# Optimization experiments

Hardware: AMD Instinct MI355X
Metric: run time of the kernel (lower is better)

Reference implementation:

```python
import jax, jax.numpy as jnp
import numpy as np

B, C, H, W = 32, 256, 32, 32
C8 = C // 8


def setup_inputs() -> dict:
    key = jax.random.key(0)
    ks = jax.random.split(key, 8)
    s = 1.0 / np.sqrt(C)
    return {
        "x": jax.random.normal(ks[0], (B, C, H, W), dtype=jnp.float32),
        "Wq": jax.random.normal(ks[1], (C8, C), dtype=jnp.float32) * s,
        "bq": jax.random.normal(ks[2], (C8,), dtype=jnp.float32) * s,
        "Wk": jax.random.normal(ks[3], (C8, C), dtype=jnp.float32) * s,
        "bk": jax.random.normal(ks[4], (C8,), dtype=jnp.float32) * s,
        "Wv": jax.random.normal(ks[5], (C, C), dtype=jnp.float32) * s,
        "bv": jax.random.normal(ks[6], (C,), dtype=jnp.float32) * s,
        "gamma": jax.random.normal(ks[7], (1,), dtype=jnp.float32) * 0.1,
    }


def reference(x, Wq, bq, Wk, bk, Wv, bv, gamma):
    b, c, h, w = x.shape
    n = h * w
    xf = x.reshape(b, c, n)  # [B, C, N]
    # 1x1 convs == per-pixel linear projections
    q = jnp.einsum('dc,bcn->bnd', Wq, xf) + bq            # [B, N, C/8]
    k = jnp.einsum('dc,bcn->bdn', Wk, xf) + bk[:, None]    # [B, C/8, N]
    v = jnp.einsum('dc,bcn->bdn', Wv, xf) + bv[:, None]    # [B, C, N]
    energy = jnp.einsum('bnd,bdm->bnm', q, k)              # [B, N, N], no scaling (as in source)
    attn = jax.nn.softmax(energy, axis=-1)                 # softmax over keys
    # out[:, :, i] = sum_j V[:, :, j] * attn[i, j]
    out = jnp.einsum('bdn,bmn->bdm', v, attn)              # [B, C, N]
    out = out.reshape(b, c, h, w)
    return gamma * out + x
```

## Files before the change

kernel.cpp:

```cpp
#include <hip/hip_runtime.h>
#include <math.h>

#define BB 32
#define CC 256
#define CQ 32
#define NN 1024

typedef short bf16x8 __attribute__((ext_vector_type(8)));
typedef float f32x4  __attribute__((ext_vector_type(4)));
typedef unsigned short u16;

__device__ __forceinline__ u16 f2bf(float f) {
    unsigned u = __float_as_uint(f);
    u = (u + 0x7FFFu + ((u >> 16) & 1u)) >> 16;
    return (u16)u;
}

__global__ void wpack_kernel(const float* __restrict__ Wq,
                             const float* __restrict__ Wk,
                             const float* __restrict__ Wv,
                             u16* __restrict__ wfrag)
{
    const int o = blockIdx.x * 256 + threadIdx.x;
    const int j    = o & 7;
    const int lane = (o >> 3) & 63;
    const int kc   = (o >> 9) & 7;
    const int rt   = o >> 12;
    const int row  = rt * 16 + (lane & 15);
    const int col  = kc * 32 + (lane >> 4) * 8 + j;
    const float v = (row < 32) ? Wq[row * 256 + col]
                  : (row < 64) ? Wk[(row - 32) * 256 + col]
                               : Wv[(row - 64) * 256 + col];
    wfrag[o] = f2bf(v);
}

struct QSmem {
    union {
        u16 xs[64][268];
        u16 osv[CC][72];
    };
    u16 osqk[64][72];
};

__global__ __launch_bounds__(256, 2) void qkv_kernel(
    const float* __restrict__ x, const u16* __restrict__ wfrag,
    const float* __restrict__ bq, const float* __restrict__ bk,
    const float* __restrict__ bv,
    u16* __restrict__ qt, u16* __restrict__ kt, u16* __restrict__ vv)
{
    __shared__ QSmem sm;
    const int b = blockIdx.y, n0 = blockIdx.x * 64;
    const int t = threadIdx.x;
    const int lane = t & 63, w = t >> 6;
    const int quad = lane >> 4, c16 = lane & 15;

    {
        const float* xb = x + (size_t)b * CC * NN + n0;
        const int n2 = 2 * (lane & 31);
        const int cr = w * 2 + (lane >> 5);
        float2 f[32];
#pragma unroll
        for (int it = 0; it < 32; ++it)
            f[it] = *(const float2*)(xb + (size_t)(it * 8 + cr) * NN + n2);
#pragma unroll
        for (int it = 0; it < 32; ++it) {
            const int c = it * 8 + cr;
            sm.xs[n2 + 0][c] = f2bf(f[it].x);
            sm.xs[n2 + 1][c] = f2bf(f[it].y);
        }
    }
    __syncthreads();

    f32x4 acc[5][4];
#pragma unroll
    for (int i = 0; i < 5; ++i)
#pragma unroll
        for (int j = 0; j < 4; ++j) acc[i][j] = (f32x4){0.f, 0.f, 0.f, 0.f};

#pragma unroll 2
    for (int k = 0; k < 8; ++k) {
        const int c0 = k * 32;
        bf16x8 wa[5], xb[4];
#pragma unroll
        for (int rs = 0; rs < 5; ++rs)
            wa[rs] = *(const bf16x8*)&wfrag[(size_t)(((w * 5 + rs) * 8 + k) * 64 + lane) * 8];
#pragma unroll
        for (int ns = 0; ns < 4; ++ns) {
            const short4 a = *(const short4*)&sm.xs[ns * 16 + c16][c0 + quad * 8];
            const short4 b2 = *(const short4*)&sm.xs[ns * 16 + c16][c0 + quad * 8 + 4];
            bf16x8 v;
            v[0] = a.x; v[1] = a.y; v[2] = a.z; v[3] = a.w;
            v[4] = b2.x; v[5] = b2.y; v[6] = b2.z; v[7] = b2.w;
            xb[ns] = v;
        }
#pragma unroll
        for (int rs = 0; rs < 5; ++rs)
#pragma unroll
            for (int ns = 0; ns < 4; ++ns)
                acc[rs][ns] = __builtin_amdgcn_mfma_f32_16x16x32_bf16(
                    wa[rs], xb[ns], acc[rs][ns], 0, 0, 0);
    }

    __syncthreads();

#pragma unroll
    for (int rs = 0; rs < 5; ++rs) {
#pragma unroll
        for (int r = 0; r < 4; ++r) {
            const int rg = w * 80 + rs * 16 + quad * 4 + r;
            const float bias = (rg < 32) ? bq[rg] : (rg < 64) ? bk[rg - 32] : bv[rg - 64];
#pragma unroll
            for (int ns = 0; ns < 4; ++ns) {
                const int n = ns * 16 + c16;
                const u16 h = f2bf(acc[rs][ns][r] + bias);
                if (rg < 64) sm.osqk[n][rg] = h;
                else         sm.osv[rg - 64][n] = h;
            }
        }
    }
    __syncthreads();

    {
        u16* dst = (w >= 2) ? kt : qt;
        const int dof = (w >= 2) ? 32 : 0;
        const int wl = w & 1;
        const size_t base = ((size_t)b * NN + n0) * CQ;
#pragma unroll
        for (int it = 0; it < 4; ++it) {
            const int o = wl * 2048 + it * 512 + lane * 8;
            const int n = o >> 5, d = o & 31;
            const bf16x8 v = *(const bf16x8*)&sm.osqk[n][d + dof];
            *(bf16x8*)&dst[base + o] = v;
        }
    }
#pragma unroll
    for (int it = 0; it < 8; ++it) {
        const int o = it * 2048 + t * 8;
        const int c = o >> 6, n = o & 63;
        const bf16x8 v = *(const bf16x8*)&sm.osv[c][n];
        *(bf16x8*)&vv[((size_t)b * CC + c) * NN + n0 + n] = v;
    }
}

__global__ __launch_bounds__(256, 2) void attn_kernel(
    const u16* __restrict__ qt, const u16* __restrict__ kt,
    const u16* __restrict__ vv, const float* __restrict__ x,
    const float* __restrict__ gamma_p, float* __restrict__ out)
{
    __shared__ u16 ps16[2][64][72];

    const int bid  = blockIdx.x;
    const int xcd  = bid & 7;
    const int slot = bid >> 3;
    const int b    = (xcd << 2) | (slot >> 4);
    const int m0   = (slot & 15) * 64;

    const int t = threadIdx.x, lane = t & 63, w = t >> 6;
    const int quad = lane >> 4, c16 = lane & 15;
    const int ch   = c16 >> 3;
    const int c7   = c16 & 7;
    const int qkey = (c16 >> 2) & 3;

    const bf16x8 qa = *(const bf16x8*)&qt[((size_t)b * NN + m0 + w * 16 + c16) * CQ + quad * 8];

    bf16x8 ones;
#pragma unroll
    for (int j = 0; j < 8; ++j) ones[j] = (short)0x3F80;

    f32x4 accO[4][4];
    f32x4 lsum[4];
#pragma unroll
    for (int i = 0; i < 4; ++i) {
        lsum[i] = (f32x4){0.f, 0.f, 0.f, 0.f};
#pragma unroll
        for (int j = 0; j < 4; ++j) accO[i][j] = (f32x4){0.f, 0.f, 0.f, 0.f};
    }

    const u16* vbase = vv + (size_t)b * CC * NN;
    const u16* kbase = kt + (size_t)b * NN * CQ;

    bf16x8 kb[4];
#pragma unroll
    for (int s = 0; s < 4; ++s)
        kb[s] = *(const bf16x8*)&kbase[(size_t)(s * 16 + c16) * CQ + quad * 8];

    bf16x8 vaA[4][2], vaB[4][2];
#pragma unroll
    for (int cs = 0; cs < 4; ++cs)
#pragma unroll
        for (int kc = 0; kc < 2; ++kc)
            vaA[cs][kc] = *(const bf16x8*)&vbase[
                (size_t)(w * 64 + cs * 16 + c16) * NN + kc * 32 + quad * 8];

    auto STEP = [&](int step, bf16x8 (&vc)[4][2], bf16x8 (&vn)[4][2]) {
        const int nbase = step * 64;
        u16* psb = &ps16[step & 1][0][0];

        f32x4 accS[4];
#pragma unroll
        for (int s = 0; s < 4; ++s)
            accS[s] = __builtin_amdgcn_mfma_f32_16x16x32_bf16(
                qa, kb[s], (f32x4){0.f, 0.f, 0.f, 0.f}, 0, 0, 0);

        const int rowb = w * 16 + quad * 4;
#pragma unroll
        for (int r = 0; r < 4; ++r)
#pragma unroll
            for (int s = 0; s < 4; ++s) {
                const int nb = (2 * s + ch) ^ quad;
                psb[(rowb + r) * 72 + nb * 8 + c7] = f2bf(__expf(accS[s][r]));
            }

        if (step < 15) {
#pragma unroll
            for (int s = 0; s < 4; ++s)
                kb[s] = *(const bf16x8*)&kbase[(size_t)(nbase + 64 + s * 16 + c16) * CQ + quad * 8];
        }

        __syncthreads();

        if (step < 15) {
#pragma unroll
            for (int cs = 0; cs < 4; ++cs)
#pragma unroll
                for (int kc = 0; kc < 2; ++kc)
                    vn[cs][kc] = *(const bf16x8*)&vbase[
                        (size_t)(w * 64 + cs * 16 + c16) * NN + nbase + 64 + kc * 32 + quad * 8];
        }

#pragma unroll
        for (int ms = 0; ms < 4; ++ms) {
            bf16x8 pb[2];
#pragma unroll
            for (int kc = 0; kc < 2; ++kc)
                pb[kc] = *(const bf16x8*)&psb[(ms * 16 + c16) * 72
                                              + (4 * kc + (quad ^ qkey)) * 8];
            lsum[ms] = __builtin_amdgcn_mfma_f32_16x16x32_bf16(ones, pb[0], lsum[ms], 0, 0, 0);
            lsum[ms] = __builtin_amdgcn_mfma_f32_16x16x32_bf16(ones, pb[1], lsum[ms], 0, 0, 0);
#pragma unroll
            for (int cs = 0; cs < 4; ++cs) {
#pragma unroll
                for (int kc = 0; kc < 2; ++kc)
                    accO[cs][ms] = __builtin_amdgcn_mfma_f32_16x16x32_bf16(
                        vc[cs][kc], pb[kc], accO[cs][ms], 0, 0, 0);
            }
        }
    };

    for (int it = 0; it < 8; ++it) {
        STEP(2 * it,     vaA, vaB);
        STEP(2 * it + 1, vaB, vaA);
    }

    const float gamma = gamma_p[0];
#pragma unroll
    for (int ms = 0; ms < 4; ++ms) {
        const float inv = gamma / lsum[ms][0];
        const int m = m0 + ms * 16 + c16;
#pragma unroll
        for (int cs = 0; cs < 4; ++cs) {
            const int cbase = w * 64 + cs * 16 + quad * 4;
#pragma unroll
            for (int r = 0; r < 4; ++r) {
                const size_t idx = ((size_t)b * CC + cbase + r) * NN + m;
                out[idx] = accO[cs][ms][r] * inv + x[idx];
            }
        }
    }
}

extern "C" void kernel_launch(void* const* d_in, const int* in_sizes, int n_in,
                              void* d_out, int out_size, void* d_ws, size_t ws_size,
                              hipStream_t stream)
{
    const float* x  = (const float*)d_in[0];
    const float* Wq = (const float*)d_in[1];
    const float* bq = (const float*)d_in[2];
    const float* Wk = (const float*)d_in[3];
    const float* bk = (const float*)d_in[4];
    const float* Wv = (const float*)d_in[5];
    const float* bv = (const float*)d_in[6];
    const float* gm = (const float*)d_in[7];
    float* out = (float*)d_out;

    u16* qt    = (u16*)d_ws;
    u16* kt    = qt + (size_t)BB * NN * CQ;
    u16* vv    = kt + (size_t)BB * NN * CQ;
    u16* wfrag = vv + (size_t)BB * CC * NN;

    wpack_kernel<<<320, 256, 0, stream>>>(Wq, Wk, Wv, wfrag);
    dim3 grid(16, BB);
    qkv_kernel<<<grid, 256, 0, stream>>>(x, wfrag, bq, bk, bv, qt, kt, vv);
    attn_kernel<<<512, 256, 0, stream>>>(qt, kt, vv, x, gm, out);
}
```

Measured before the change: 155.9 us.

## Split attention block across 8 waves and pack bf16 conversions

Doubles the attention kernel's block to 512 threads so each wave owns 32 output channels instead of 64, and the S-tile computation is split across waves by key half. The row sum is computed by one wave per row group and shared through LDS. Exp results are now converted with the packed v_cvt_pk_bf16_f32 instruction. The V register double-buffering is dropped in favour of loading V at the start of each step. This reduces register pressure to raise occupancy, at the cost of more sync participants and less explicit prefetch.

```diff
diff --git a/kernel.cpp b/kernel.cpp
--- a/kernel.cpp
+++ b/kernel.cpp
@@ -14,6 +14,12 @@
     unsigned u = __float_as_uint(f);
     u = (u + 0x7FFFu + ((u >> 16) & 1u)) >> 16;
     return (u16)u;
+}
+
+__device__ __forceinline__ unsigned cvt_pk_bf16(float lo, float hi) {
+    unsigned r;
+    asm("v_cvt_pk_bf16_f32 %0, %1, %2" : "=v"(r) : "v"(lo), "v"(hi));
+    return r;
 }
 
 __global__ void wpack_kernel(const float* __restrict__ Wq,
@@ -142,12 +148,13 @@
     }
 }
 
-__global__ __launch_bounds__(256, 2) void attn_kernel(
+__global__ __launch_bounds__(512, 4) void attn_kernel(
     const u16* __restrict__ qt, const u16* __restrict__ kt,
     const u16* __restrict__ vv, const float* __restrict__ x,
     const float* __restrict__ gamma_p, float* __restrict__ out)
 {
     __shared__ u16 ps16[2][64][72];
+    __shared__ float lsh[64];
 
     const int bid  = blockIdx.x;
     const int xcd  = bid & 7;
@@ -160,106 +167,106 @@
     const int ch   = c16 >> 3;
     const int c7   = c16 & 7;
     const int qkey = (c16 >> 2) & 3;
-
-    const bf16x8 qa = *(const bf16x8*)&qt[((size_t)b * NN + m0 + w * 16 + c16) * CQ + quad * 8];
+    const int sm   = w & 3;
+    const int sh   = w >> 2;
+    const int ms0  = w & 3;
+
+    const bf16x8 qa = *(const bf16x8*)&qt[((size_t)b * NN + m0 + sm * 16 + c16) * CQ + quad * 8];
 
     bf16x8 ones;
 #pragma unroll
     for (int j = 0; j < 8; ++j) ones[j] = (short)0x3F80;
 
-    f32x4 accO[4][4];
-    f32x4 lsum[4];
-#pragma unroll
-    for (int i = 0; i < 4; ++i) {
-        lsum[i] = (f32x4){0.f, 0.f, 0.f, 0.f};
-#pragma unroll
-        for (int j = 0; j < 4; ++j) accO[i][j] = (f32x4){0.f, 0.f, 0.f, 0.f};
-    }
+    f32x4 accO[2][4];
+    f32x4 lsum = (f32x4){0.f, 0.f, 0.f, 0.f};
+#pragma unroll
+    for (int cs = 0; cs < 2; ++cs)
+#pragma unroll
+        for (int j = 0; j < 4; ++j) accO[cs][j] = (f32x4){0.f, 0.f, 0.f, 0.f};
 
     const u16* vbase = vv + (size_t)b * CC * NN;
     const u16* kbase = kt + (size_t)b * NN * CQ;
 
-    bf16x8 kb[4];
-#pragma unroll
-    for (int s = 0; s < 4; ++s)
-        kb[s] = *(const bf16x8*)&kbase[(size_t)(s * 16 + c16) * CQ + quad * 8];
-
-    bf16x8 vaA[4][2], vaB[4][2];
-#pragma unroll
-    for (int cs = 0; cs < 4; ++cs)
-#pragma unroll
-        for (int kc = 0; kc < 2; ++kc)
-            vaA[cs][kc] = *(const bf16x8*)&vbase[
-                (size_t)(w * 64 + cs * 16 + c16) * NN + kc * 32 + quad * 8];
-
-    auto STEP = [&](int step, bf16x8 (&vc)[4][2], bf16x8 (&vn)[4][2]) {
+    bf16x8 kb[2];
+#pragma unroll
+    for (int s = 0; s < 2; ++s)
+        kb[s] = *(const bf16x8*)&kbase[(size_t)(sh * 32 + s * 16 + c16) * CQ + quad * 8];
+
+    for (int step = 0; step < 16; ++step) {
         const int nbase = step * 64;
         u16* psb = &ps16[step & 1][0][0];
 
-        f32x4 accS[4];
-#pragma unroll
-        for (int s = 0; s < 4; ++s)
+        bf16x8 va[2][2];
+#pragma unroll
+        for (int cs = 0; cs < 2; ++cs)
+#pragma unroll
+            for (int kc = 0; kc < 2; ++kc)
+                va[cs][kc] = *(const bf16x8*)&vbase[
+                    (size_t)(w * 32 + cs * 16 + c16) * NN + nbase + kc * 32 + quad * 8];
+
+        f32x4 accS[2];
+#pragma unroll
+        for (int s = 0; s < 2; ++s)
             accS[s] = __builtin_amdgcn_mfma_f32_16x16x32_bf16(
                 qa, kb[s], (f32x4){0.f, 0.f, 0.f, 0.f}, 0, 0, 0);
 
-        const int rowb = w * 16 + quad * 4;
-#pragma unroll
-        for (int r = 0; r < 4; ++r)
-#pragma unroll
-            for (int s = 0; s < 4; ++s) {
-                const int nb = (2 * s + ch) ^ quad;
-                psb[(rowb + r) * 72 + nb * 8 + c7] = f2bf(__expf(accS[s][r]));
+        const int rowb = sm * 16 + quad * 4;
+#pragma unroll
+        for (int s = 0; s < 2; ++s) {
+            const int nb = (sh * 4 + 2 * s + ch) ^ quad;
+            u16* pw = &psb[rowb * 72 + nb * 8 + c7];
+            const float e0 = __expf(accS[s][0]);
+            const float e1 = __expf(accS[s][1]);
+            const float e2 = __expf(accS[s][2]);
+            const float e3 = __expf(accS[s][3]);
+            const unsigned p01 = cvt_pk_bf16(e0, e1);
+            const unsigned p23 = cvt_pk_bf16(e2, e3);
+            pw[0]       = (u16)p01;
+            pw[72]      = (u16)(p01 >> 16);
+            pw[144]     = (u16)p23;
+            pw[216]     = (u16)(p23 >> 16);
+        }
+
+        if (step < 15) {
+#pragma unroll
+            for (int s = 0; s < 2; ++s)
+                kb[s] = *(const bf16x8*)&kbase[
+                    (size_t)(nbase + 64 + sh * 32 + s * 16 + c16) * CQ + quad * 8];
+        }
+
+        __syncthreads();
+
+#pragma unroll
+        for (int msi = 0; msi < 4; ++msi) {
+            bf16x8 pb[2];
+#pragma unroll
+            for (int kc = 0; kc < 2; ++kc)
+                pb[kc] = *(const bf16x8*)&psb[(msi * 16 + c16) * 72
+                                              + (4 * kc + (quad ^ qkey)) * 8];
+            if (msi == ms0) {
+                lsum = __builtin_amdgcn_mfma_f32_16x16x32_bf16(ones, pb[0], lsum, 0, 0, 0);
+                lsum = __builtin_amdgcn_mfma_f32_16x16x32_bf16(ones, pb[1], lsum, 0, 0, 0);
             }
-
-        if (step < 15) {
-#pragma unroll
-            for (int s = 0; s < 4; ++s)
-                kb[s] = *(const bf16x8*)&kbase[(size_t)(nbase + 64 + s * 16 + c16) * CQ + quad * 8];
-        }
-
-        __syncthreads();
-
-        if (step < 15) {
-#pragma unroll
-            for (int cs = 0; cs < 4; ++cs)
+#pragma unroll
+            for (int cs = 0; cs < 2; ++cs)
 #pragma unroll
                 for (int kc = 0; kc < 2; ++kc)
-                    vn[cs][kc] = *(const bf16x8*)&vbase[
-                        (size_t)(w * 64 + cs * 16 + c16) * NN + nbase + 64 + kc * 32 + quad * 8];
-        }
-
-#pragma unroll
-        for (int ms = 0; ms < 4; ++ms) {
-            bf16x8 pb[2];
-#pragma unroll
-            for (int kc = 0; kc < 2; ++kc)
-                pb[kc] = *(const bf16x8*)&psb[(ms * 16 + c16) * 72
-                                              + (4 * kc + (quad ^ qkey)) * 8];
-            lsum[ms] = __builtin_amdgcn_mfma_f32_16x16x32_bf16(ones, pb[0], lsum[ms], 0, 0, 0);
-            lsum[ms] = __builtin_amdgcn_mfma_f32_16x16x32_bf16(ones, pb[1], lsum[ms], 0, 0, 0);
-#pragma unroll
-            for (int cs = 0; cs < 4; ++cs) {
-#pragma unroll
-                for (int kc = 0; kc < 2; ++kc)
-                    accO[cs][ms] = __builtin_amdgcn_mfma_f32_16x16x32_bf16(
-                        vc[cs][kc], pb[kc], accO[cs][ms], 0, 0, 0);
-            }
-        }
-    };
-
-    for (int it = 0; it < 8; ++it) {
-        STEP(2 * it,     vaA, vaB);
-        STEP(2 * it + 1, vaB, vaA);
-    }
+                    accO[cs][msi] = __builtin_amdgcn_mfma_f32_16x16x32_bf16(
+                        va[cs][kc], pb[kc], accO[cs][msi], 0, 0, 0);
+        }
+    }
+
+    if (sh == 0 && quad == 0) lsh[ms0 * 16 + c16] = lsum[0];
+    __syncthreads();
 
     const float gamma = gamma_p[0];
 #pragma unroll
     for (int ms = 0; ms < 4; ++ms) {
-        const float inv = gamma / lsum[ms][0];
+        const float inv = gamma / lsh[ms * 16 + c16];
         const int m = m0 + ms * 16 + c16;
 #pragma unroll
-        for (int cs = 0; cs < 4; ++cs) {
-            const int cbase = w * 64 + cs * 16 + quad * 4;
+        for (int cs = 0; cs < 2; ++cs) {
+            const int cbase = w * 32 + cs * 16 + quad * 4;
 #pragma unroll
             for (int r = 0; r < 4; ++r) {
                 const size_t idx = ((size_t)b * CC + cbase + r) * NN + m;
@@ -291,5 +298,5 @@
     wpack_kernel<<<320, 256, 0, stream>>>(Wq, Wk, Wv, wfrag);
     dim3 grid(16, BB);
     qkv_kernel<<<grid, 256, 0, stream>>>(x, wfrag, bq, bk, bv, qt, kt, vv);
-    attn_kernel<<<512, 256, 0, stream>>>(qt, kt, vv, x, gm, out);
-}
+    attn_kernel<<<512, 512, 0, stream>>>(qt, kt, vv, x, gm, out);
+}
```

New measurement: 152.9 us. No clear change (-2.0%).
